# Optimization experiments

Hardware: AMD Instinct MI355X
Metric: run time of the kernel (lower is better)

## Reference

```python
import jax, jax.numpy as jnp
import numpy as np

H = 36   # num_heads
D = 32   # head_dim
C = 1152 # hidden_size (== H*D)


def setup_inputs() -> dict:
    key = jax.random.key(0)
    k1, k2, k3, k4 = jax.random.split(key, 4)
    B, N = 4, 8192
    x = jax.random.normal(k1, (B, N, C), dtype=jnp.float32)
    # torch Linear(hidden, 3*inner, bias=False): we store as (in, out) for x @ W
    W_qkv = jax.random.normal(k2, (C, 3 * H * D), dtype=jnp.float32) * (1.0 / np.sqrt(C))
    W_out = jax.random.normal(k3, (H * D, C), dtype=jnp.float32) * (1.0 / np.sqrt(H * D))
    b_out = jax.random.normal(k4, (C,), dtype=jnp.float32) * 0.01
    return {"x": x, "W_qkv": W_qkv, "W_out": W_out, "b_out": b_out}


def reference(x, W_qkv, W_out, b_out):
    B, N, _ = x.shape
    qkv = (x @ W_qkv).reshape(B, N, 3, H, D)
    q = jax.nn.relu(qkv[:, :, 0])  # (B,N,H,D)
    k = jax.nn.relu(qkv[:, :, 1])
    v = qkv[:, :, 2]
    # kv state: per-head (D,D) outer-product sum over tokens
    kv = jnp.einsum('bnhd,bnhe->bhde', k, v)        # (B,H,D,D)
    out = jnp.einsum('bnhd,bhde->bnhe', q, kv)      # (B,N,H,D)
    k_sum = k.sum(axis=1)                            # (B,H,D)
    denom = jnp.einsum('bnhd,bhd->bnh', q, k_sum)[..., None] + 1e-6
    out = (out / denom).reshape(B, N, H * D)
    return out @ W_out + b_out
```

## Files before the change

### kernel.cpp

```cpp
#include <hip/hip_runtime.h>
#include <stdint.h>


#define HH 36
#define DD 32
#define CC 1152
#define NB 4
#define NN 8192
#define M_TOT (NB * NN)
#define N1 (3 * HH * DD)
#define HD (HH * DD)
#define HPB 3
#define KVSPLIT 32

typedef __attribute__((ext_vector_type(8))) short bf16x8;
typedef __attribute__((ext_vector_type(4))) float f32x4;

__device__ __forceinline__ uint16_t f2b(float f) {
  union { float f; uint32_t u; } v; v.f = f;
  uint32_t u = v.u;
  return (uint16_t)((u + 0x7fffu + ((u >> 16) & 1u)) >> 16);
}
__device__ __forceinline__ float uasf(uint32_t u) {
  union { uint32_t u; float f; } v; v.u = u; return v.f;
}
__device__ __forceinline__ void unpack8v(uint4 u, f32x4& lo, f32x4& hi) {
  lo[0] = uasf(u.x << 16); lo[1] = uasf(u.x & 0xffff0000u);
  lo[2] = uasf(u.y << 16); lo[3] = uasf(u.y & 0xffff0000u);
  hi[0] = uasf(u.z << 16); hi[1] = uasf(u.z & 0xffff0000u);
  hi[2] = uasf(u.w << 16); hi[3] = uasf(u.w & 0xffff0000u);
}

#define GLOAD16(g, l)                                                        \
  __builtin_amdgcn_global_load_lds(                                          \
      (const __attribute__((address_space(1))) void*)(g),                    \
      (__attribute__((address_space(3))) void*)(l), 16, 0, 0)

__device__ __forceinline__ int swz_off(int row, int col) {
  int off = ((row >> 4) * 2 + (col >> 5)) * 1024 + (row & 15) * 64 + (col & 31) * 2;
  return off ^ (((off >> 9) & 1) << 5);
}
__device__ __forceinline__ void stage_decode(int d, int& row, int& col) {
  int lin = d ^ (((d >> 9) & 1) << 5);
  int s = lin >> 10;
  row = (s >> 1) * 16 + ((lin >> 6) & 15);
  col = (s & 1) * 32 + ((lin >> 1) & 31);
}

__global__ void zero_kernel(float* __restrict__ p, int n) {
  int i = blockIdx.x * blockDim.x + threadIdx.x;
  if (i < n) p[i] = 0.f;
}

__global__ void convert_kernel(const float* __restrict__ in, uint16_t* __restrict__ out, int n4) {
  int i = blockIdx.x * blockDim.x + threadIdx.x;
  if (i >= n4) return;
  float4 v = ((const float4*)in)[i];
  ushort4 o;
  o.x = f2b(v.x); o.y = f2b(v.y); o.z = f2b(v.z); o.w = f2b(v.w);
  ((ushort4*)out)[i] = o;
}

__global__ void transpose_convert_kernel(const float* __restrict__ in, uint16_t* __restrict__ out,
                                         int R, int Cc) {
  __shared__ uint16_t tile[32][33];
  int c0 = blockIdx.x * 32, r0 = blockIdx.y * 32;
  int tx = threadIdx.x & 31, ty = threadIdx.x >> 5;
#pragma unroll
  for (int i = 0; i < 4; i++) {
    int r = ty + i * 8;
    tile[r][tx] = f2b(in[(size_t)(r0 + r) * Cc + c0 + tx]);
  }
  __syncthreads();
#pragma unroll
  for (int i = 0; i < 4; i++) {
    int c = ty + i * 8;
    out[(size_t)(c0 + c) * R + r0 + tx] = tile[tx][c];
  }
}

template <int EPI, int NREAL>
__global__ __launch_bounds__(512, 2)
void gemm256_kernel(const uint16_t* __restrict__ A, const uint16_t* __restrict__ BT,
                    uint16_t* __restrict__ outb, float* __restrict__ outf,
                    const float* __restrict__ bias) {
  constexpr int K = 1152;
  constexpr int NTT = K / 64;
  constexpr int NTx = (EPI == 0) ? 14 : 5;
  __shared__ uint16_t lds[2][4][8192];

  const int flat = blockIdx.y * NTx + blockIdx.x;
  const int xcd = flat & 7, sg = flat >> 3;
  const int n0 = (sg % NTx) * 256;
  const int m0 = ((sg / NTx) * 8 + xcd) * 256;
  const int tid = threadIdx.x;
  const int lane = tid & 63, w = tid >> 6;
  const int wm = w >> 2, wn = w & 3;
  const int l15 = lane & 15, q4 = lane >> 4;

  int r0, c0, r1, c1;
  stage_decode(tid * 16, r0, c0);
  stage_decode(tid * 16 + 8192, r1, c1);
  const size_t go0 = (size_t)r0 * K + c0;
  const size_t go1 = (size_t)r1 * K + c1;
  const uint16_t* A0p = A + (size_t)m0 * K;
  const uint16_t* A1p = A + (size_t)(m0 + 128) * K;
  const uint16_t* B0p = BT + (size_t)n0 * K;
  const uint16_t* B1p = BT + (size_t)(n0 + 128) * K;
  const int stl = w * 512;

#define STAGE(bp, kt, slot)                                                  \
  {                                                                          \
    const uint16_t* _g = (bp) + (size_t)(kt) * 64;                           \
    GLOAD16(_g + go0, (slot) + stl);                                         \
    GLOAD16(_g + go1, (slot) + 4096 + stl);                                  \
  }
#define LGKM0()                                           \
  asm volatile("s_waitcnt lgkmcnt(0)" ::: "memory");      \
  __builtin_amdgcn_sched_barrier(0)

  f32x4 acc[8][4] = {};
  bf16x8 a[4][2], b[2][2][2];

  STAGE(B1p, 0, &lds[0][3][0]);
  STAGE(A1p, 0, &lds[0][1][0]);
  STAGE(A0p, 0, &lds[0][0][0]);
  STAGE(B0p, 0, &lds[0][2][0]);
  STAGE(B1p, 1, &lds[1][3][0]);
  STAGE(A1p, 1, &lds[1][1][0]);
  asm volatile("s_waitcnt vmcnt(4)" ::: "memory");
  __builtin_amdgcn_s_barrier();

#pragma unroll 2
  for (int T = 0; T < NTT; T++) {
    const int cur = T & 1;
    const int tn = (T + 1 < NTT) ? T + 1 : NTT - 1;
    const int tn2 = (T + 2 < NTT) ? T + 2 : NTT - 1;
    const uint16_t* sA = &lds[cur][wm][0];
    const uint16_t* sB = &lds[cur][2 + (wn >> 1)][0];
#pragma unroll
    for (int i = 0; i < 4; i++)
#pragma unroll
      for (int kk = 0; kk < 2; kk++)
        a[i][kk] = *(const bf16x8*)((const char*)sA +
            swz_off(i * 16 + l15, kk * 32 + q4 * 8));
#pragma unroll
    for (int j = 0; j < 2; j++)
#pragma unroll
      for (int kk = 0; kk < 2; kk++)
        b[0][j][kk] = *(const bf16x8*)((const char*)sB +
            swz_off((wn & 1) * 64 + j * 16 + l15, kk * 32 + q4 * 8));
    STAGE(A0p, tn, &lds[cur ^ 1][0][0]);
    __builtin_amdgcn_s_barrier();
    LGKM0();
    __builtin_amdgcn_s_setprio(1);
#pragma unroll
    for (int i = 0; i < 4; i++)
#pragma unroll
      for (int j = 0; j < 2; j++)
#pragma unroll
        for (int kk = 0; kk < 2; kk++)
          acc[i][j] = __builtin_amdgcn_mfma_f32_16x16x32_bf16(
              a[i][kk], b[0][j][kk], acc[i][j], 0, 0, 0);
    __builtin_amdgcn_s_setprio(0);
    __builtin_amdgcn_s_barrier();
#pragma unroll
    for (int j = 0; j < 2; j++)
#pragma unroll
      for (int kk = 0; kk < 2; kk++)
        b[1][j][kk] = *(const bf16x8*)((const char*)sB +
            swz_off((wn & 1) * 64 + 32 + j * 16 + l15, kk * 32 + q4 * 8));
    STAGE(B0p, tn, &lds[cur ^ 1][2][0]);
    __builtin_amdgcn_s_barrier();
    LGKM0();
    __builtin_amdgcn_s_setprio(1);
#pragma unroll
    for (int i = 0; i < 4; i++)
#pragma unroll
      for (int j = 0; j < 2; j++)
#pragma unroll
        for (int kk = 0; kk < 2; kk++)
          acc[i][2 + j] = __builtin_amdgcn_mfma_f32_16x16x32_bf16(
              a[i][kk], b[1][j][kk], acc[i][2 + j], 0, 0, 0);
    __builtin_amdgcn_s_setprio(0);
    __builtin_amdgcn_s_barrier();
#pragma unroll
    for (int i = 0; i < 4; i++)
#pragma unroll
      for (int kk = 0; kk < 2; kk++)
        a[i][kk] = *(const bf16x8*)((const char*)sA +
            swz_off(64 + i * 16 + l15, kk * 32 + q4 * 8));
    STAGE(B1p, tn2, &lds[cur][3][0]);
    __builtin_amdgcn_s_barrier();
    LGKM0();
    __builtin_amdgcn_s_setprio(1);
#pragma unroll
    for (int i = 0; i < 4; i++)
#pragma unroll
      for (int j = 0; j < 2; j++)
#pragma unroll
        for (int kk = 0; kk < 2; kk++)
          acc[4 + i][2 + j] = __builtin_amdgcn_mfma_f32_16x16x32_bf16(
              a[i][kk], b[1][j][kk], acc[4 + i][2 + j], 0, 0, 0);
    __builtin_amdgcn_s_setprio(0);
    __builtin_amdgcn_s_barrier();
    STAGE(A1p, tn2, &lds[cur][1][0]);
    __builtin_amdgcn_s_barrier();
    LGKM0();
    __builtin_amdgcn_s_setprio(1);
#pragma unroll
    for (int i = 0; i < 4; i++)
#pragma unroll
      for (int j = 0; j < 2; j++)
#pragma unroll
        for (int kk = 0; kk < 2; kk++)
          acc[4 + i][j] = __builtin_amdgcn_mfma_f32_16x16x32_bf16(
              a[i][kk], b[0][j][kk], acc[4 + i][j], 0, 0, 0);
    __builtin_amdgcn_s_setprio(0);
    asm volatile("s_waitcnt vmcnt(4)" ::: "memory");
    __builtin_amdgcn_s_barrier();
  }
  asm volatile("s_waitcnt vmcnt(0)" ::: "memory");
#pragma unroll
  for (int mi = 0; mi < 8; mi++) {
    const int row = m0 + wm * 128 + mi * 16 + q4 * 4;
#pragma unroll
    for (int nj = 0; nj < 4; nj++) {
      const int col = n0 + wn * 64 + nj * 16 + l15;
      if (col < NREAL) {
#pragma unroll
        for (int r = 0; r < 4; r++) {
          float v = acc[mi][nj][r];
          if (EPI == 0) {
            if (col < 2 * HD) v = fmaxf(v, 0.f);
            outb[(size_t)(row + r) * NREAL + col] = f2b(v);
          } else {
            outf[(size_t)(row + r) * NREAL + col] = v + bias[col];
          }
        }
      }
    }
  }
#undef STAGE
#undef LGKM0
}

__global__ __launch_bounds__(64)
void kv_kernel(const uint16_t* __restrict__ qkvb, float* __restrict__ kvT, float* __restrict__ ksum) {
  __shared__ float kb[32][40];
  __shared__ float vb[32][40];
  const int bh = blockIdx.x / KVSPLIT;
  const int sp = blockIdx.x % KVSPLIT;
  const int b = bh / HH, h = bh % HH;
  const int t = threadIdx.x;
  const int d0 = (t >> 3) * 4, e0 = (t & 7) * 4;
  const int m0 = b * NN + sp * (NN / KVSPLIT);
  const size_t koff = (size_t)HD + h * DD;
  const size_t voff = (size_t)2 * HD + h * DD;
  float acc[4][4] = {};
  float ks[4] = {};
  const int srow = t >> 1, sseg = (t & 1) * 16;
  for (int c = 0; c < NN / KVSPLIT; c += 32) {
    const uint16_t* kp = qkvb + (size_t)(m0 + c + srow) * N1 + koff + sseg;
    const uint16_t* vp = qkvb + (size_t)(m0 + c + srow) * N1 + voff + sseg;
    uint4 kr0 = *(const uint4*)kp;
    uint4 kr1 = *(const uint4*)(kp + 8);
    uint4 vr0 = *(const uint4*)vp;
    uint4 vr1 = *(const uint4*)(vp + 8);
    f32x4 klo, khi, klo2, khi2, vlo, vhi, vlo2, vhi2;
    unpack8v(kr0, klo, khi); unpack8v(kr1, klo2, khi2);
    unpack8v(vr0, vlo, vhi); unpack8v(vr1, vlo2, vhi2);
    __syncthreads();
    *(f32x4*)&kb[srow][sseg + 0] = klo;  *(f32x4*)&kb[srow][sseg + 4] = khi;
    *(f32x4*)&kb[srow][sseg + 8] = klo2; *(f32x4*)&kb[srow][sseg + 12] = khi2;
    *(f32x4*)&vb[srow][sseg + 0] = vlo;  *(f32x4*)&vb[srow][sseg + 4] = vhi;
    *(f32x4*)&vb[srow][sseg + 8] = vlo2; *(f32x4*)&vb[srow][sseg + 12] = vhi2;
    __syncthreads();
#pragma unroll 8
    for (int n = 0; n < 32; n++) {
      f32x4 kd = *(const f32x4*)&kb[n][d0];
      f32x4 ve = *(const f32x4*)&vb[n][e0];
#pragma unroll
      for (int i = 0; i < 4; i++)
#pragma unroll
        for (int j = 0; j < 4; j++) acc[i][j] += kd[i] * ve[j];
      if ((t & 7) == 0) {
#pragma unroll
        for (int i = 0; i < 4; i++) ks[i] += kd[i];
      }
    }
  }
#pragma unroll
  for (int i = 0; i < 4; i++)
#pragma unroll
    for (int j = 0; j < 4; j++)
      atomicAdd(&kvT[(size_t)bh * 1024 + (e0 + j) * DD + d0 + i], acc[i][j]);
  if ((t & 7) == 0) {
#pragma unroll
    for (int i = 0; i < 4; i++) atomicAdd(&ksum[bh * DD + d0 + i], ks[i]);
  }
}

__global__ __launch_bounds__(256)
void attn_kernel(const uint16_t* __restrict__ qkvb, const float* __restrict__ kvT,
                 const float* __restrict__ ksum, uint16_t* __restrict__ attn) {
  const int t = threadIdx.x;
  const int lane = t & 63, w = t >> 6;
  const int mbase = blockIdx.x * 256 + w * 64;
  const int b = mbase >> 13;
  const int e = lane & 31, dh = lane >> 5;
  const int h0 = blockIdx.y * HPB;
  for (int hh = 0; hh < HPB; hh++) {
    const int h = h0 + hh;
    const int bh = b * HH + h;
    const float* kvp = kvT + (size_t)bh * 1024 + e * DD + dh * 16;
    f32x4 kva = *(const f32x4*)(kvp + 0);
    f32x4 kvb2 = *(const f32x4*)(kvp + 4);
    f32x4 kvc = *(const f32x4*)(kvp + 8);
    f32x4 kvd = *(const f32x4*)(kvp + 12);
    const float* ksp = ksum + bh * DD + dh * 16;
    f32x4 ksa = *(const f32x4*)(ksp + 0);
    f32x4 ksb = *(const f32x4*)(ksp + 4);
    f32x4 ksc = *(const f32x4*)(ksp + 8);
    f32x4 ksd = *(const f32x4*)(ksp + 12);
#pragma unroll 4
    for (int r = 0; r < 64; r++) {
      const int m = mbase + r;
      const uint16_t* qp = qkvb + (size_t)m * N1 + h * DD + dh * 16;
      uint4 q0 = *(const uint4*)qp;
      uint4 q1 = *(const uint4*)(qp + 8);
      f32x4 qa, qb2, qc, qd;
      unpack8v(q0, qa, qb2);
      unpack8v(q1, qc, qd);
      float o = 0.f, den = 0.f;
#pragma unroll
      for (int ii = 0; ii < 4; ii++) {
        o += qa[ii] * kva[ii];  den += qa[ii] * ksa[ii];
        o += qb2[ii] * kvb2[ii]; den += qb2[ii] * ksb[ii];
        o += qc[ii] * kvc[ii];  den += qc[ii] * ksc[ii];
        o += qd[ii] * kvd[ii];  den += qd[ii] * ksd[ii];
      }
      o += __shfl_xor(o, 32);
      den += __shfl_xor(den, 32);
      float res = o / (den + 1e-6f);
      if (dh == 0) attn[(size_t)m * HD + h * DD + e] = f2b(res);
    }
  }
}

extern "C" void kernel_launch(void* const* d_in, const int* in_sizes, int n_in,
                              void* d_out, int out_size, void* d_ws, size_t ws_size,
                              hipStream_t stream) {
  const float* x = (const float*)d_in[0];
  const float* Wqkv = (const float*)d_in[1];
  const float* Wout = (const float*)d_in[2];
  const float* bout = (const float*)d_in[3];
  float* y = (float*)d_out;
  char* ws = (char*)d_ws;
  uint16_t* xb = (uint16_t*)ws;
  uint16_t* wqkvT = (uint16_t*)(ws + 75497472);
  uint16_t* qkvb = (uint16_t*)(ws + 83755008);
  float* kvT = (float*)(ws + 310247424);
  float* ksum = (float*)(ws + 310837248);
  uint16_t* woutT = qkvb;
  uint16_t* attn = xb;

  zero_kernel<<<(152064 + 255) / 256, 256, 0, stream>>>(kvT, 152064);
  convert_kernel<<<(M_TOT * CC / 4) / 256, 256, 0, stream>>>(x, xb, M_TOT * CC / 4);
  transpose_convert_kernel<<<dim3(N1 / 32, CC / 32), 256, 0, stream>>>(Wqkv, wqkvT, CC, N1);
  gemm256_kernel<0, N1><<<dim3(14, 128), 512, 0, stream>>>(xb, wqkvT, qkvb, nullptr, nullptr);
  kv_kernel<<<144 * KVSPLIT, 64, 0, stream>>>(qkvb, kvT, ksum);
  attn_kernel<<<dim3(M_TOT / 256, HH / HPB), 256, 0, stream>>>(qkvb, kvT, ksum, attn);
  transpose_convert_kernel<<<dim3(CC / 32, CC / 32), 256, 0, stream>>>(Wout, woutT, CC, CC);
  gemm256_kernel<1, HD><<<dim3(5, 128), 512, 0, stream>>>(attn, woutT, nullptr, y, bout);
}
```

Before: 987.1 us.

## Restructure GEMM main loop into full double-buffered prefetch of next tile fragments

Reworks the bf16 MFMA GEMM main loop so both K-tiles are staged before entry and the A/B register fragments for the next tile are read from the alternate LDS buffer while the current tile's MFMAs run. Global stages are now issued in pairs per phase instead of one per phase. The loop drops from 8 barriers per iteration to 4, and it uses raw s_barrier asm with no sched_barrier fences. The aim is to cut synchronisation stalls and hide LDS read latency behind MFMA work. The cost is higher register pressure from the extra fragment buffers, and the hand-placed waitcnt counts now carry correctness risk.

Result: slower. 1.086 ms (+10.0%).

```diff
diff --git a/kernel.cpp b/kernel.cpp
--- a/kernel.cpp
+++ b/kernel.cpp
@@ -115,44 +115,53 @@
     GLOAD16(_g + go0, (slot) + stl);                                         \
     GLOAD16(_g + go1, (slot) + 4096 + stl);                                  \
   }
-#define LGKM0()                                           \
-  asm volatile("s_waitcnt lgkmcnt(0)" ::: "memory");      \
-  __builtin_amdgcn_sched_barrier(0)
+#define RD(ptr, row, col) \
+  (*(const bf16x8*)((const char*)(ptr) + swz_off((row), (col))))
+#define BAR() asm volatile("s_barrier" ::: "memory")
+#define LGKM0() asm volatile("s_waitcnt lgkmcnt(0)" ::: "memory")
 
   f32x4 acc[8][4] = {};
-  bf16x8 a[4][2], b[2][2][2];
-
+  bf16x8 aL[4][2], aH[4][2], bl[2][2], bh[2][2];
+  const int bro = (wn & 1) * 64;
+
+  STAGE(A0p, 0, &lds[0][0][0]);
+  STAGE(A1p, 0, &lds[0][1][0]);
+  STAGE(B0p, 0, &lds[0][2][0]);
   STAGE(B1p, 0, &lds[0][3][0]);
-  STAGE(A1p, 0, &lds[0][1][0]);
-  STAGE(A0p, 0, &lds[0][0][0]);
-  STAGE(B0p, 0, &lds[0][2][0]);
+  STAGE(B0p, 1, &lds[1][2][0]);
   STAGE(B1p, 1, &lds[1][3][0]);
+  STAGE(A0p, 1, &lds[1][0][0]);
   STAGE(A1p, 1, &lds[1][1][0]);
-  asm volatile("s_waitcnt vmcnt(4)" ::: "memory");
-  __builtin_amdgcn_s_barrier();
-
-#pragma unroll 2
+  asm volatile("s_waitcnt vmcnt(8)" ::: "memory");
+  BAR();
+  {
+    const uint16_t* sA0 = &lds[0][wm][0];
+    const uint16_t* sB0 = &lds[0][2 + (wn >> 1)][0];
+#pragma unroll
+    for (int i = 0; i < 4; i++)
+#pragma unroll
+      for (int kk = 0; kk < 2; kk++)
+        aL[i][kk] = RD(sA0, i * 16 + l15, kk * 32 + q4 * 8);
+#pragma unroll
+    for (int j = 0; j < 2; j++)
+#pragma unroll
+      for (int kk = 0; kk < 2; kk++)
+        bl[j][kk] = RD(sB0, bro + j * 16 + l15, kk * 32 + q4 * 8);
+  }
+
+#pragma unroll 1
   for (int T = 0; T < NTT; T++) {
     const int cur = T & 1;
-    const int tn = (T + 1 < NTT) ? T + 1 : NTT - 1;
-    const int tn2 = (T + 2 < NTT) ? T + 2 : NTT - 1;
+    const int t2 = (T + 2 < NTT) ? T + 2 : NTT - 1;
     const uint16_t* sA = &lds[cur][wm][0];
     const uint16_t* sB = &lds[cur][2 + (wn >> 1)][0];
-#pragma unroll
-    for (int i = 0; i < 4; i++)
-#pragma unroll
-      for (int kk = 0; kk < 2; kk++)
-        a[i][kk] = *(const bf16x8*)((const char*)sA +
-            swz_off(i * 16 + l15, kk * 32 + q4 * 8));
+    const uint16_t* sAn = &lds[cur ^ 1][wm][0];
+    const uint16_t* sBn = &lds[cur ^ 1][2 + (wn >> 1)][0];
 #pragma unroll
     for (int j = 0; j < 2; j++)
 #pragma unroll
       for (int kk = 0; kk < 2; kk++)
-        b[0][j][kk] = *(const bf16x8*)((const char*)sB +
-            swz_off((wn & 1) * 64 + j * 16 + l15, kk * 32 + q4 * 8));
-    STAGE(A0p, tn, &lds[cur ^ 1][0][0]);
-    __builtin_amdgcn_s_barrier();
-    LGKM0();
+        bh[j][kk] = RD(sB, bro + 32 + j * 16 + l15, kk * 32 + q4 * 8);
     __builtin_amdgcn_s_setprio(1);
 #pragma unroll
     for (int i = 0; i < 4; i++)
@@ -161,18 +170,17 @@
 #pragma unroll
         for (int kk = 0; kk < 2; kk++)
           acc[i][j] = __builtin_amdgcn_mfma_f32_16x16x32_bf16(
-              a[i][kk], b[0][j][kk], acc[i][j], 0, 0, 0);
+              aL[i][kk], bl[j][kk], acc[i][j], 0, 0, 0);
     __builtin_amdgcn_s_setprio(0);
-    __builtin_amdgcn_s_barrier();
-#pragma unroll
-    for (int j = 0; j < 2; j++)
-#pragma unroll
-      for (int kk = 0; kk < 2; kk++)
-        b[1][j][kk] = *(const bf16x8*)((const char*)sB +
-            swz_off((wn & 1) * 64 + 32 + j * 16 + l15, kk * 32 + q4 * 8));
-    STAGE(B0p, tn, &lds[cur ^ 1][2][0]);
-    __builtin_amdgcn_s_barrier();
     LGKM0();
+    BAR();
+#pragma unroll
+    for (int i = 0; i < 4; i++)
+#pragma unroll
+      for (int kk = 0; kk < 2; kk++)
+        aH[i][kk] = RD(sA, 64 + i * 16 + l15, kk * 32 + q4 * 8);
+    STAGE(B0p, t2, &lds[cur][2][0]);
+    STAGE(B1p, t2, &lds[cur][3][0]);
     __builtin_amdgcn_s_setprio(1);
 #pragma unroll
     for (int i = 0; i < 4; i++)
@@ -181,18 +189,18 @@
 #pragma unroll
         for (int kk = 0; kk < 2; kk++)
           acc[i][2 + j] = __builtin_amdgcn_mfma_f32_16x16x32_bf16(
-              a[i][kk], b[1][j][kk], acc[i][2 + j], 0, 0, 0);
+              aL[i][kk], bh[j][kk], acc[i][2 + j], 0, 0, 0);
     __builtin_amdgcn_s_setprio(0);
-    __builtin_amdgcn_s_barrier();
-#pragma unroll
-    for (int i = 0; i < 4; i++)
-#pragma unroll
-      for (int kk = 0; kk < 2; kk++)
-        a[i][kk] = *(const bf16x8*)((const char*)sA +
-            swz_off(64 + i * 16 + l15, kk * 32 + q4 * 8));
-    STAGE(B1p, tn2, &lds[cur][3][0]);
-    __builtin_amdgcn_s_barrier();
     LGKM0();
+    asm volatile("s_waitcnt vmcnt(4)" ::: "memory");
+    BAR();
+#pragma unroll
+    for (int i = 0; i < 4; i++)
+#pragma unroll
+      for (int kk = 0; kk < 2; kk++)
+        aL[i][kk] = RD(sAn, i * 16 + l15, kk * 32 + q4 * 8);
+    STAGE(A0p, t2, &lds[cur][0][0]);
+    STAGE(A1p, t2, &lds[cur][1][0]);
     __builtin_amdgcn_s_setprio(1);
 #pragma unroll
     for (int i = 0; i < 4; i++)
@@ -201,12 +209,9 @@
 #pragma unroll
         for (int kk = 0; kk < 2; kk++)
           acc[4 + i][2 + j] = __builtin_amdgcn_mfma_f32_16x16x32_bf16(
-              a[i][kk], b[1][j][kk], acc[4 + i][2 + j], 0, 0, 0);
+              aH[i][kk], bh[j][kk], acc[4 + i][2 + j], 0, 0, 0);
     __builtin_amdgcn_s_setprio(0);
-    __builtin_amdgcn_s_barrier();
-    STAGE(A1p, tn2, &lds[cur][1][0]);
-    __builtin_amdgcn_s_barrier();
-    LGKM0();
+    BAR();
     __builtin_amdgcn_s_setprio(1);
 #pragma unroll
     for (int i = 0; i < 4; i++)
@@ -215,10 +220,14 @@
 #pragma unroll
         for (int kk = 0; kk < 2; kk++)
           acc[4 + i][j] = __builtin_amdgcn_mfma_f32_16x16x32_bf16(
-              a[i][kk], b[0][j][kk], acc[4 + i][j], 0, 0, 0);
+              aH[i][kk], bl[j][kk], acc[4 + i][j], 0, 0, 0);
     __builtin_amdgcn_s_setprio(0);
-    asm volatile("s_waitcnt vmcnt(4)" ::: "memory");
-    __builtin_amdgcn_s_barrier();
+#pragma unroll
+    for (int j = 0; j < 2; j++)
+#pragma unroll
+      for (int kk = 0; kk < 2; kk++)
+        bl[j][kk] = RD(sBn, bro + j * 16 + l15, kk * 32 + q4 * 8);
+    BAR();
   }
   asm volatile("s_waitcnt vmcnt(0)" ::: "memory");
 #pragma unroll
@@ -242,6 +251,8 @@
     }
   }
 #undef STAGE
+#undef RD
+#undef BAR
 #undef LGKM0
 }
 
```

## Use 128x128 tile GEMM for output projection and relax LDS waits in main GEMM

Applied to the files above, without the earlier changes.

Replaces the 256x256-tile gemm for the output projection (N=1152, which wasted a partial tile with 5 column tiles) with a new 128x128-tile, 256-thread kernel with XCD-aware block mapping and swizzled LDS. Also tweaks the QKV GEMM pipeline by removing sched_barriers, adding a partial lgkmcnt wait and dropping one full LDS wait. The new kernel is single-buffered with two syncthreads per k-step, so it has less latency hiding, and the removed wait may rely on earlier waits for correctness.

Result: faster. 948.5 us (-3.9%).

```diff
diff --git a/kernel.cpp b/kernel.cpp
--- a/kernel.cpp
+++ b/kernel.cpp
@@ -115,9 +115,9 @@
     GLOAD16(_g + go0, (slot) + stl);                                         \
     GLOAD16(_g + go1, (slot) + 4096 + stl);                                  \
   }
-#define LGKM0()                                           \
-  asm volatile("s_waitcnt lgkmcnt(0)" ::: "memory");      \
-  __builtin_amdgcn_sched_barrier(0)
+#define RD(ptr, row, col) \
+  (*(const bf16x8*)((const char*)(ptr) + swz_off((row), (col))))
+#define LGKM0() asm volatile("s_waitcnt lgkmcnt(0)" ::: "memory")
 
   f32x4 acc[8][4] = {};
   bf16x8 a[4][2], b[2][2][2];
@@ -138,19 +138,19 @@
     const int tn2 = (T + 2 < NTT) ? T + 2 : NTT - 1;
     const uint16_t* sA = &lds[cur][wm][0];
     const uint16_t* sB = &lds[cur][2 + (wn >> 1)][0];
+    const int bro = (wn & 1) * 64;
 #pragma unroll
     for (int i = 0; i < 4; i++)
 #pragma unroll
       for (int kk = 0; kk < 2; kk++)
-        a[i][kk] = *(const bf16x8*)((const char*)sA +
-            swz_off(i * 16 + l15, kk * 32 + q4 * 8));
+        a[i][kk] = RD(sA, i * 16 + l15, kk * 32 + q4 * 8);
 #pragma unroll
     for (int j = 0; j < 2; j++)
 #pragma unroll
       for (int kk = 0; kk < 2; kk++)
-        b[0][j][kk] = *(const bf16x8*)((const char*)sB +
-            swz_off((wn & 1) * 64 + j * 16 + l15, kk * 32 + q4 * 8));
+        b[0][j][kk] = RD(sB, bro + j * 16 + l15, kk * 32 + q4 * 8);
     STAGE(A0p, tn, &lds[cur ^ 1][0][0]);
+    asm volatile("s_waitcnt lgkmcnt(8)" ::: "memory");
     __builtin_amdgcn_s_barrier();
     LGKM0();
     __builtin_amdgcn_s_setprio(1);
@@ -168,8 +168,7 @@
     for (int j = 0; j < 2; j++)
 #pragma unroll
       for (int kk = 0; kk < 2; kk++)
-        b[1][j][kk] = *(const bf16x8*)((const char*)sB +
-            swz_off((wn & 1) * 64 + 32 + j * 16 + l15, kk * 32 + q4 * 8));
+        b[1][j][kk] = RD(sB, bro + 32 + j * 16 + l15, kk * 32 + q4 * 8);
     STAGE(B0p, tn, &lds[cur ^ 1][2][0]);
     __builtin_amdgcn_s_barrier();
     LGKM0();
@@ -188,8 +187,7 @@
     for (int i = 0; i < 4; i++)
 #pragma unroll
       for (int kk = 0; kk < 2; kk++)
-        a[i][kk] = *(const bf16x8*)((const char*)sA +
-            swz_off(64 + i * 16 + l15, kk * 32 + q4 * 8));
+        a[i][kk] = RD(sA, 64 + i * 16 + l15, kk * 32 + q4 * 8);
     STAGE(B1p, tn2, &lds[cur][3][0]);
     __builtin_amdgcn_s_barrier();
     LGKM0();
@@ -206,7 +204,6 @@
     __builtin_amdgcn_s_barrier();
     STAGE(A1p, tn2, &lds[cur][1][0]);
     __builtin_amdgcn_s_barrier();
-    LGKM0();
     __builtin_amdgcn_s_setprio(1);
 #pragma unroll
     for (int i = 0; i < 4; i++)
@@ -242,7 +239,83 @@
     }
   }
 #undef STAGE
+#undef RD
 #undef LGKM0
+}
+
+template <int EPI, int NC>
+__global__ __launch_bounds__(256, 4)
+void gemm_bf16_kernel(const uint16_t* __restrict__ A, const uint16_t* __restrict__ BT,
+                      uint16_t* __restrict__ outb, float* __restrict__ outf,
+                      const float* __restrict__ bias, int K) {
+  constexpr int NT = NC / 128;
+  __shared__ uint16_t As[128 * 64];
+  __shared__ uint16_t Bs[128 * 64];
+  const int flat = blockIdx.y * NT + blockIdx.x;
+  const int xcd = flat & 7;
+  const int s = flat >> 3;
+  const int n0 = (s % NT) * 128;
+  const int m0 = ((s / NT) * 8 + xcd) * 128;
+  const int t = threadIdx.x;
+  const int lane = t & 63, w = t >> 6;
+  const int wr = w >> 1, wc = w & 1;
+  const int l15 = lane & 15, q4 = lane >> 4;
+  f32x4 acc[4][4] = {};
+
+  const int srow = w * 32 + (lane >> 3);
+  const int sseg = ((lane & 7) ^ (lane >> 3)) * 8;
+  const uint16_t* Ag = A + (size_t)(m0 + srow) * K + sseg;
+  const uint16_t* Bg = BT + (size_t)(n0 + srow) * K + sseg;
+  uint16_t* lA = &As[(w * 32) * 64];
+  uint16_t* lB = &Bs[(w * 32) * 64];
+
+  for (int k0 = 0; k0 < K; k0 += 64) {
+    __syncthreads();
+#pragma unroll
+    for (int i = 0; i < 4; i++) {
+      GLOAD16(Ag + k0 + (size_t)(i * 8) * K, lA + i * 8 * 64);
+      GLOAD16(Bg + k0 + (size_t)(i * 8) * K, lB + i * 8 * 64);
+    }
+    __syncthreads();
+#pragma unroll
+    for (int kk = 0; kk < 2; kk++) {
+      bf16x8 af[4], bfr[4];
+      const int sbase = (kk * 4 + q4);
+#pragma unroll
+      for (int i = 0; i < 4; i++) {
+        const int row = wr * 64 + i * 16 + l15;
+        af[i] = *(const bf16x8*)&As[row * 64 + (sbase ^ (l15 & 7)) * 8];
+      }
+#pragma unroll
+      for (int j = 0; j < 4; j++) {
+        const int row = wc * 64 + j * 16 + l15;
+        bfr[j] = *(const bf16x8*)&Bs[row * 64 + (sbase ^ (l15 & 7)) * 8];
+      }
+#pragma unroll
+      for (int i = 0; i < 4; i++)
+#pragma unroll
+        for (int j = 0; j < 4; j++)
+          acc[i][j] = __builtin_amdgcn_mfma_f32_16x16x32_bf16(af[i], bfr[j], acc[i][j], 0, 0, 0);
+    }
+  }
+#pragma unroll
+  for (int i = 0; i < 4; i++) {
+#pragma unroll
+    for (int j = 0; j < 4; j++) {
+      int col = n0 + wc * 64 + j * 16 + l15;
+#pragma unroll
+      for (int r = 0; r < 4; r++) {
+        int row = m0 + wr * 64 + i * 16 + q4 * 4 + r;
+        float v = acc[i][j][r];
+        if (EPI == 0) {
+          if (col < 2 * HD) v = fmaxf(v, 0.f);
+          outb[(size_t)row * NC + col] = f2b(v);
+        } else {
+          outf[(size_t)row * NC + col] = v + bias[col];
+        }
+      }
+    }
+  }
 }
 
 __global__ __launch_bounds__(64)
@@ -372,5 +445,5 @@
   kv_kernel<<<144 * KVSPLIT, 64, 0, stream>>>(qkvb, kvT, ksum);
   attn_kernel<<<dim3(M_TOT / 256, HH / HPB), 256, 0, stream>>>(qkvb, kvT, ksum, attn);
   transpose_convert_kernel<<<dim3(CC / 32, CC / 32), 256, 0, stream>>>(Wout, woutT, CC, CC);
-  gemm256_kernel<1, HD><<<dim3(5, 128), 512, 0, stream>>>(attn, woutT, nullptr, y, bout);
-}
+  gemm_bf16_kernel<1, CC><<<dim3(CC / 128, M_TOT / 128), 256, 0, stream>>>(attn, woutT, nullptr, y, bout, CC);
+}
```
